# Optimization experiments

Hardware: AMD Instinct MI355X
Metric: run time of the kernel (lower is better)

Reference implementation:

```python
import jax, jax.numpy as jnp
import numpy as np

DIM = 512
HEADS = 8
DHEAD = 64
WIN = 128
QK_SCALE = 8.0
LN_EPS = 1e-5


def setup_inputs() -> dict:
    key = jax.random.key(0)
    ks = jax.random.split(key, 5)
    B, N = 8, 4096
    x = jax.random.normal(ks[0], (B, N, DIM), jnp.float32)
    w_qkv = jax.random.normal(ks[1], (3 * HEADS * DHEAD, DIM), jnp.float32) * 0.02
    w_out = jax.random.normal(ks[2], (DIM, HEADS * DHEAD), jnp.float32) * 0.02
    b_out = jnp.zeros((DIM,), jnp.float32)
    w_ff1 = jax.random.normal(ks[3], (4 * DIM, DIM), jnp.float32) * 0.02
    w_ff2 = jax.random.normal(ks[4], (DIM, 4 * DIM), jnp.float32) * 0.02
    return {
        'x': x, 'w_qkv': w_qkv,
        'q_scale': jnp.ones((DHEAD,), jnp.float32),
        'k_scale': jnp.ones((DHEAD,), jnp.float32),
        'w_out': w_out, 'b_out': b_out,
        'ln1_g': jnp.ones((DIM,), jnp.float32), 'ln1_b': jnp.zeros((DIM,), jnp.float32),
        'ff_ln_g': jnp.ones((DIM,), jnp.float32), 'ff_ln_b': jnp.zeros((DIM,), jnp.float32),
        'w_ff1': w_ff1, 'w_ff2': w_ff2,
    }


def _ln(x, g, b):
    m = jnp.mean(x, axis=-1, keepdims=True)
    v = jnp.mean((x - m) ** 2, axis=-1, keepdims=True)
    return (x - m) * jax.lax.rsqrt(v + LN_EPS) * g + b


def _l2norm(t):
    return t / jnp.clip(jnp.linalg.norm(t, axis=-1, keepdims=True), 1e-12)


def _rotary(t, pos):
    # t: (B, H, N, DHEAD); standard (non-xpos) rotary, half-split style
    inv_freq = 1.0 / (10000.0 ** (jnp.arange(0, DHEAD, 2, dtype=jnp.float32) / DHEAD))
    freqs = pos[:, None] * inv_freq                      # (N, DHEAD/2)
    emb = jnp.concatenate([freqs, freqs], axis=-1)       # (N, DHEAD)
    cos, sin = jnp.cos(emb), jnp.sin(emb)
    t1, t2 = t[..., : DHEAD // 2], t[..., DHEAD // 2:]
    rot = jnp.concatenate([-t2, t1], axis=-1)
    return t * cos + rot * sin


def reference(x, w_qkv, q_scale, k_scale, w_out, b_out, ln1_g, ln1_b,
              ff_ln_g, ff_ln_b, w_ff1, w_ff2):
    B, N, D = x.shape
    nw = N // WIN

    # ---- LocalMHA (prenorm, qk-rmsnorm, sliding window, causal) ----
    h = _ln(x, ln1_g, ln1_b)
    qkv = h @ w_qkv.T                                    # (B, N, 3*H*DHEAD)
    q, k, v = jnp.split(qkv, 3, axis=-1)

    def to_heads(t):
        return t.reshape(B, N, HEADS, DHEAD).transpose(0, 2, 1, 3)  # (B,H,N,d)

    q, k, v = to_heads(q), to_heads(k), to_heads(v)
    q = _l2norm(q) * q_scale
    k = _l2norm(k) * k_scale
    pos = jnp.arange(N, dtype=jnp.float32)
    q = _rotary(q, pos)
    k = _rotary(k, pos)

    # bucket into windows; keys/values look back one window
    bq = q.reshape(B, HEADS, nw, WIN, DHEAD)
    bk = k.reshape(B, HEADS, nw, WIN, DHEAD)
    bv = v.reshape(B, HEADS, nw, WIN, DHEAD)

    def look_back(t):
        prev = jnp.concatenate([jnp.zeros_like(t[:, :, :1]), t[:, :, :-1]], axis=2)
        return jnp.concatenate([prev, t], axis=3)

    kk, vv = look_back(bk), look_back(bv)

    qpos = jnp.arange(N, dtype=jnp.int32).reshape(nw, WIN)
    kprev = jnp.concatenate([jnp.full((1, WIN), -1, jnp.int32), qpos[:-1]], axis=0)
    kpos = jnp.concatenate([kprev, qpos], axis=1)
    mask = (qpos[:, :, None] >= kpos[:, None, :]) & (kpos[:, None, :] >= 0)

    sim = jnp.einsum('bhnid,bhnjd->bhnij', bq, kk) * QK_SCALE
    sim = jnp.where(mask, sim, -1e9)
    attn = jax.nn.softmax(sim, axis=-1)
    out = jnp.einsum('bhnij,bhnjd->bhnid', attn, vv)
    out = out.reshape(B, HEADS, N, DHEAD).transpose(0, 2, 1, 3).reshape(B, N, HEADS * DHEAD)
    x = x + out @ w_out.T + b_out

    # ---- FeedForward: LN -> Linear(4D, no bias) -> GELU -> Linear(D, no bias) ----
    hf = _ln(x, ff_ln_g, ff_ln_b)
    ff = jax.nn.gelu(hf @ w_ff1.T, approximate=False) @ w_ff2.T
    return x + ff
```

## Files before the change

kernel.cpp:

```cpp
#include <hip/hip_runtime.h>
#include <cstdint>
#include <cstddef>

typedef __bf16 bf16;
typedef __bf16 bf16x8 __attribute__((ext_vector_type(8)));
typedef float f32x4 __attribute__((ext_vector_type(4)));

#define DEV static __device__ __forceinline__

constexpr int BATCH = 8;
constexpr int SEQ = 4096;
constexpr int DIM = 512;
constexpr int HEADS = 8;
constexpr int DH = 64;
constexpr int WIN = 128;
constexpr int NW = SEQ / WIN;
constexpr int TOK = BATCH * SEQ;
constexpr float EPS = 1e-5f;

constexpr size_t R_EL   = (size_t)TOK * DIM;
constexpr size_t C_QKV  = 0;
constexpr size_t C_WOUT = 786432;
constexpr size_t C_WF1  = 1048576;
constexpr size_t C_WF2  = 2097152;
constexpr size_t C_SM   = 3145728;
constexpr size_t P_EL   = 3148416;

DEV void gload_lds16(const void* g, void* l) {
  __builtin_amdgcn_global_load_lds((__attribute__((address_space(1))) void*)g,
                                   (__attribute__((address_space(3))) void*)l,
                                   16, 0, 0);
}

DEV f32x4 mfma16(bf16x8 a, bf16x8 b, f32x4 c) {
  return __builtin_amdgcn_mfma_f32_16x16x32_bf16(a, b, c, 0, 0, 0);
}

struct SrcPtrs { const void* p[12]; };

DEV void copy8(const void* src, long si, bf16* dst, bool f32) {
  if (f32) {
    const float4* s = (const float4*)((const float*)src + si);
    float4 a = s[0], b = s[1];
    bf16x8 o;
    o[0] = (bf16)a.x; o[1] = (bf16)a.y; o[2] = (bf16)a.z; o[3] = (bf16)a.w;
    o[4] = (bf16)b.x; o[5] = (bf16)b.y; o[6] = (bf16)b.z; o[7] = (bf16)b.w;
    *(bf16x8*)dst = o;
  } else {
    *(bf16x8*)dst = *(const bf16x8*)((const bf16*)src + si);
  }
}

__global__ __launch_bounds__(256) void ingest_kernel(SrcPtrs sp, bf16* cano) {
  const bool f32 = (((const unsigned short*)sp.p[2])[0] == 0);
  const long e = (long)threadIdx.x * 8;
  int b = blockIdx.x;
  if (b < 384)  { long o = (long)b * 2048 + e; copy8(sp.p[1], o, cano + C_QKV + o, f32); return; }
  b -= 384;
  if (b < 128)  { long o = (long)b * 2048 + e; copy8(sp.p[4], o, cano + C_WOUT + o, f32); return; }
  b -= 128;
  if (b < 512)  { long o = (long)b * 2048 + e; copy8(sp.p[10], o, cano + C_WF1 + o, f32); return; }
  b -= 512;
  if (b < 512)  { long o = (long)b * 2048 + e; copy8(sp.p[11], o, cano + C_WF2 + o, f32); return; }
  b -= 512;
  const long o = (long)b * 2048 + e;
  if (o >= 2688) return;
  const void* src; long si;
  if      (o < 64)   { src = sp.p[2]; si = o; }
  else if (o < 128)  { src = sp.p[3]; si = o - 64; }
  else if (o < 640)  { src = sp.p[5]; si = o - 128; }
  else if (o < 1152) { src = sp.p[6]; si = o - 640; }
  else if (o < 1664) { src = sp.p[7]; si = o - 1152; }
  else if (o < 2176) { src = sp.p[8]; si = o - 1664; }
  else               { src = sp.p[9]; si = o - 2176; }
  copy8(src, si, cano + C_SM + o, f32);
}

__global__ __launch_bounds__(256) void ln_kernel(const void* __restrict__ in,
                                                 const bf16* __restrict__ gg,
                                                 const bf16* __restrict__ bb,
                                                 bf16* __restrict__ out,
                                                 const unsigned short* __restrict__ probe,
                                                 int raw) {
  const int wave = threadIdx.x >> 6, lane = threadIdx.x & 63;
  const int row = blockIdx.x * 4 + wave;
  const size_t base = (size_t)row * DIM + lane * 8;
  float f[8];
  if (raw && probe[0] == 0) {
    const float4* p = (const float4*)((const float*)in + base);
    float4 a = p[0], bq = p[1];
    f[0] = a.x; f[1] = a.y; f[2] = a.z; f[3] = a.w;
    f[4] = bq.x; f[5] = bq.y; f[6] = bq.z; f[7] = bq.w;
  } else {
    bf16x8 v = *(const bf16x8*)((const bf16*)in + base);
#pragma unroll
    for (int i = 0; i < 8; ++i) f[i] = (float)v[i];
  }
  float s = 0.f, sq = 0.f;
#pragma unroll
  for (int i = 0; i < 8; ++i) { s += f[i]; sq += f[i] * f[i]; }
#pragma unroll
  for (int m = 32; m; m >>= 1) { s += __shfl_xor(s, m); sq += __shfl_xor(sq, m); }
  const float mean = s * (1.0f / DIM);
  const float var = fmaxf(sq * (1.0f / DIM) - mean * mean, 0.0f);
  const float rs = rsqrtf(var + EPS);
  bf16x8 gv = *(const bf16x8*)(gg + lane * 8);
  bf16x8 bv = *(const bf16x8*)(bb + lane * 8);
  bf16x8 o;
#pragma unroll
  for (int i = 0; i < 8; ++i) o[i] = (bf16)((f[i] - mean) * rs * (float)gv[i] + (float)bv[i]);
  *(bf16x8*)((bf16*)out + base) = o;
}

template <int MODE>
__global__ __launch_bounds__(256) void gemm_bt(const bf16* __restrict__ A,
                                               const bf16* __restrict__ Bw,
                                               bf16* __restrict__ O0, bf16* __restrict__ O1,
                                               bf16* __restrict__ O2,
                                               float* __restrict__ Of,
                                               const void* __restrict__ Xraw,
                                               const bf16* __restrict__ Xb,
                                               const bf16* __restrict__ bias,
                                               const unsigned short* __restrict__ probe,
                                               int K, int bstride, int ostride, int gx) {
  __shared__ __align__(16) bf16 smem[2 * 128 * 32];
  bf16* As = smem;
  bf16* Bs = smem + 4096;
  const int tid = threadIdx.x;
  const int wave = tid >> 6, lane = tid & 63;
  const int l15 = lane & 15, quad = lane >> 4;
  const int id = blockIdx.x;
  const int per = gx * 8;
  const int tM = ((id / per) * 8 + (id & 7)) * 128;
  const int tN = ((id % per) >> 3) * 128;
  const int wM = (wave >> 1) * 64, wN = (wave & 1) * 64;
  f32x4 acc[4][4];
  const f32x4 z = {0.f, 0.f, 0.f, 0.f};
#pragma unroll
  for (int i = 0; i < 4; ++i)
#pragma unroll
    for (int j = 0; j < 4; ++j) acc[i][j] = z;

  for (int k0 = 0; k0 < K; k0 += 32) {
    __syncthreads();
#pragma unroll
    for (int t = 0; t < 2; ++t) {
      const int c = tid + t * 256;
      const int row = c >> 2, cc = (c & 3) * 8;
      gload_lds16(A + (size_t)(tM + row) * K + k0 + cc, &As[c * 8]);
      gload_lds16(Bw + (size_t)(tN + row) * bstride + k0 + cc, &Bs[c * 8]);
    }
    __syncthreads();
    bf16x8 aF[4], bF[4];
#pragma unroll
    for (int i = 0; i < 4; ++i) aF[i] = *(const bf16x8*)&As[(wM + i * 16 + l15) * 32 + quad * 8];
#pragma unroll
    for (int j = 0; j < 4; ++j) bF[j] = *(const bf16x8*)&Bs[(wN + j * 16 + l15) * 32 + quad * 8];
#pragma unroll
    for (int i = 0; i < 4; ++i)
#pragma unroll
      for (int j = 0; j < 4; ++j) acc[i][j] = mfma16(aF[i], bF[j], acc[i][j]);
  }

  if constexpr (MODE == 0) {
    __syncthreads();
    bf16* ob = smem + wave * 1152;
    const int colbase = tN + wN;
    const int which = colbase >> 9;
    const int head = (colbase >> 6) & 7;
    bf16* dst = which == 0 ? O0 : (which == 1 ? O1 : O2);
    const int ch = lane & 7;
    float scv[8], invf[8];
    if (which < 2) {
      const bf16* sc = which ? bias : Xb;
      bf16x8 s8 = *(const bf16x8*)(sc + ch * 8);
#pragma unroll
      for (int u = 0; u < 8; ++u) {
        scv[u] = (float)s8[u] * (which == 0 ? 8.0f : 1.0f);
        invf[u] = exp2f(-(float)((ch & 3) * 8 + u) * (13.287712379549449f / 32.0f));
      }
    }
#pragma unroll
    for (int i = 0; i < 4; ++i) {
#pragma unroll
      for (int j = 0; j < 4; ++j)
#pragma unroll
        for (int r = 0; r < 4; ++r)
          ob[(quad * 4 + r) * 72 + j * 16 + l15] = (bf16)acc[i][j][r];
#pragma unroll
      for (int t = 0; t < 2; ++t) {
        const int rr = t * 8 + (lane >> 3);
        const int rowg = tM + wM + i * 16 + rr;
        bf16x8 ov = *(const bf16x8*)&ob[rr * 72 + ch * 8];
        float f[8];
#pragma unroll
        for (int u = 0; u < 8; ++u) f[u] = (float)ov[u];
        if (which < 2) {
          float ss = 0.f;
#pragma unroll
          for (int u = 0; u < 8; ++u) ss += f[u] * f[u];
          ss += __shfl_xor(ss, 1); ss += __shfl_xor(ss, 2); ss += __shfl_xor(ss, 4);
          const float rs = 1.0f / fmaxf(sqrtf(ss), 1e-12f);
#pragma unroll
          for (int u = 0; u < 8; ++u) f[u] *= rs * scv[u];
          float pf[8];
#pragma unroll
          for (int u = 0; u < 8; ++u) pf[u] = __shfl_xor(f[u], 4);
          const float pos = (float)(rowg & (SEQ - 1));
#pragma unroll
          for (int u = 0; u < 8; ++u) {
            float sn, cs;
            __sincosf(pos * invf[u], &sn, &cs);
            const float rot = (ch < 4) ? -pf[u] : pf[u];
            f[u] = f[u] * cs + rot * sn;
          }
        }
        bf16x8 o8;
#pragma unroll
        for (int u = 0; u < 8; ++u) o8[u] = (bf16)f[u];
        const int bb = rowg >> 12, n = rowg & (SEQ - 1);
        *(bf16x8*)(dst + ((size_t)(bb * HEADS + head) * SEQ + n) * DH + ch * 8) = o8;
      }
    }
    return;
  }

  if constexpr (MODE == 1 || MODE == 2) {
    __syncthreads();
    bf16* ob = smem + wave * 1152;
    const int ch = lane & 7;
    bf16x8 bias8;
    bool xf32 = false;
    if constexpr (MODE == 1) {
      bias8 = *(const bf16x8*)(bias + tN + wN + ch * 8);
      xf32 = (probe[0] == 0);
    }
#pragma unroll
    for (int i = 0; i < 4; ++i) {
#pragma unroll
      for (int j = 0; j < 4; ++j)
#pragma unroll
        for (int r = 0; r < 4; ++r)
          ob[(quad * 4 + r) * 72 + j * 16 + l15] = (bf16)acc[i][j][r];
#pragma unroll
      for (int t = 0; t < 2; ++t) {
        const int rr = t * 8 + (lane >> 3);
        const int rowg = tM + wM + i * 16 + rr;
        bf16x8 ov = *(const bf16x8*)&ob[rr * 72 + ch * 8];
        bf16x8 o8;
        if constexpr (MODE == 1) {
          const size_t idx = (size_t)rowg * DIM + tN + wN + ch * 8;
          float xr[8];
          if (xf32) {
            const float4* xp = (const float4*)((const float*)Xraw + idx);
            float4 a = xp[0], bq = xp[1];
            xr[0] = a.x; xr[1] = a.y; xr[2] = a.z; xr[3] = a.w;
            xr[4] = bq.x; xr[5] = bq.y; xr[6] = bq.z; xr[7] = bq.w;
          } else {
            bf16x8 xv = *(const bf16x8*)((const bf16*)Xraw + idx);
#pragma unroll
            for (int u = 0; u < 8; ++u) xr[u] = (float)xv[u];
          }
#pragma unroll
          for (int u = 0; u < 8; ++u) o8[u] = (bf16)((float)ov[u] + xr[u] + (float)bias8[u]);
          *(bf16x8*)(O0 + idx) = o8;
        } else {
#pragma unroll
          for (int u = 0; u < 8; ++u) {
            const float v = (float)ov[u];
            o8[u] = (bf16)(0.5f * v * (1.0f + erff(v * 0.7071067811865476f)));
          }
          *(bf16x8*)(O0 + (size_t)rowg * ostride + tN + wN + ch * 8) = o8;
        }
      }
    }
    return;
  }

#pragma unroll
  for (int i = 0; i < 4; ++i) {
    const int rbase = tM + wM + i * 16 + quad * 4;
#pragma unroll
    for (int j = 0; j < 4; ++j) {
      const int col = tN + wN + j * 16 + l15;
#pragma unroll
      for (int r = 0; r < 4; ++r) {
        const int row = rbase + r;
        const float v = acc[i][j][r];
        if constexpr (MODE == 3) {
          const size_t idx = (size_t)row * DIM + col;
          Of[idx] = v + (float)Xb[idx];
        } else if constexpr (MODE == 4) {
          const size_t idx = (size_t)row * DIM + col;
          Of[idx] = v + Of[idx];
        }
      }
    }
  }
}

__global__ __launch_bounds__(256, 3) void attn_kernel(const bf16* __restrict__ q,
                                                      const bf16* __restrict__ k,
                                                      const bf16* __restrict__ v,
                                                      bf16* __restrict__ ao) {
  __shared__ __align__(16) bf16 kv[256 * 72];
  __shared__ __align__(16) bf16 pbuf[4][16 * 136];
  const int w = blockIdx.x, h = blockIdx.y, b = blockIdx.z;
  const int tid = threadIdx.x;
  const int wv = tid >> 6, lane = tid & 63;
  const int l15 = lane & 15, quad = lane >> 4;
  const size_t bh = (size_t)b * HEADS + h;
  const bf16* qb = q + bh * SEQ * DH;
  const bf16* kb = k + bh * SEQ * DH;
  const bf16* vb = v + bh * SEQ * DH;
  const int t0 = (w - 1) * WIN;

#pragma unroll
  for (int it = 0; it < 8; ++it) {
    const int c = it * 256 + tid;
    const int tok = c >> 3, ch = c & 7;
    int gt = t0 + tok; gt = gt < 0 ? 0 : gt;
    *(bf16x8*)&kv[tok * 72 + ch * 8] = *(const bf16x8*)(kb + (size_t)gt * DH + ch * 8);
  }
  bf16x8 aQ[2][2];
#pragma unroll
  for (int qt = 0; qt < 2; ++qt) {
    const int qtok = w * WIN + wv * 32 + qt * 16 + l15;
#pragma unroll
    for (int ks = 0; ks < 2; ++ks)
      aQ[qt][ks] = *(const bf16x8*)(qb + (size_t)qtok * DH + ks * 32 + quad * 8);
  }
  int gtv = t0 + tid; gtv = gtv < 0 ? 0 : gtv;
  bf16x8 vld[8];
#pragma unroll
  for (int dg = 0; dg < 8; ++dg)
    vld[dg] = *(const bf16x8*)(vb + (size_t)gtv * DH + dg * 8);
  __syncthreads();

  bf16x8 aP[2][8];
#pragma unroll
  for (int qt = 0; qt < 2; ++qt) {
    f32x4 sreg[16];
#pragma unroll
    for (int nt = 0; nt < 16; ++nt) {
      f32x4 a = {0.f, 0.f, 0.f, 0.f};
#pragma unroll
      for (int ks = 0; ks < 2; ++ks) {
        bf16x8 bK = *(const bf16x8*)&kv[(nt * 16 + l15) * 72 + ks * 32 + quad * 8];
        a = mfma16(aQ[qt][ks], bK, a);
      }
      sreg[nt] = a;
    }
    const int qlb = wv * 32 + qt * 16 + quad * 4;
    float rinv[4];
#pragma unroll
    for (int r = 0; r < 4; ++r) {
      const int ql = qlb + r;
      float sum = 0.f;
#pragma unroll
      for (int nt = 0; nt < 16; ++nt) {
        const int j = nt * 16 + l15;
        const bool valid = (nt < 8) ? (w > 0) : (ql >= j - WIN);
        const float p = valid ? __expf(sreg[nt][r]) : 0.0f;
        sreg[nt][r] = p;
        sum += p;
      }
#pragma unroll
      for (int m = 8; m; m >>= 1) sum += __shfl_xor(sum, m);
      rinv[r] = 1.0f / sum;
    }
#pragma unroll
    for (int half = 0; half < 2; ++half) {
#pragma unroll
      for (int ntw = 0; ntw < 8; ++ntw)
#pragma unroll
        for (int r = 0; r < 4; ++r)
          pbuf[wv][(quad * 4 + r) * 136 + ntw * 16 + l15] =
              (bf16)(sreg[half * 8 + ntw][r] * rinv[r]);
#pragma unroll
      for (int kk = 0; kk < 4; ++kk)
        aP[qt][half * 4 + kk] = *(const bf16x8*)&pbuf[wv][l15 * 136 + kk * 32 + quad * 8];
    }
  }
  __syncthreads();

#pragma unroll
  for (int dg = 0; dg < 8; ++dg)
#pragma unroll
    for (int i = 0; i < 8; ++i)
      kv[(dg * 8 + i) * 264 + tid] = vld[dg][i];
  __syncthreads();

#pragma unroll
  for (int qt = 0; qt < 2; ++qt) {
#pragma unroll
    for (int dt = 0; dt < 4; ++dt) {
      f32x4 o = {0.f, 0.f, 0.f, 0.f};
#pragma unroll
      for (int ks2 = 0; ks2 < 8; ++ks2) {
        bf16x8 bV = *(const bf16x8*)&kv[(dt * 16 + l15) * 264 + ks2 * 32 + quad * 8];
        o = mfma16(aP[qt][ks2], bV, o);
      }
#pragma unroll
      for (int r = 0; r < 4; ++r)
        pbuf[wv][(quad * 4 + r) * 136 + dt * 16 + l15] = (bf16)o[r];
    }
#pragma unroll
    for (int t = 0; t < 2; ++t) {
      const int rr = t * 8 + (lane >> 3), ch = lane & 7;
      bf16x8 ov = *(const bf16x8*)&pbuf[wv][rr * 136 + ch * 8];
      const int tok = w * WIN + wv * 32 + qt * 16 + rr;
      *(bf16x8*)(ao + ((size_t)b * SEQ + tok) * DIM + h * DH + ch * 8) = ov;
    }
  }
}

extern "C" void kernel_launch(void* const* d_in, const int* in_sizes, int n_in,
                              void* d_out, int out_size, void* d_ws, size_t ws_size,
                              hipStream_t stream) {
  (void)in_sizes; (void)n_in; (void)out_size;
  float* out = (float*)d_out;
  bf16* cano = (bf16*)d_ws;
  const unsigned short* probe = (const unsigned short*)d_in[2];

  SrcPtrs sp;
  for (int i = 0; i < 12; ++i) sp.p[i] = d_in[i];

  bf16* slot0 = cano + P_EL;
  bf16* slot1 = cano + P_EL + R_EL;
  bf16* slot2 = cano + P_EL + 2 * R_EL;
  bf16* slot3 = cano + P_EL + 3 * R_EL;

  const bf16* qsc  = cano + C_SM + 0;
  const bf16* ksc  = cano + C_SM + 64;
  const bf16* bout = cano + C_SM + 128;
  const bf16* l1g  = cano + C_SM + 640;
  const bf16* l1b  = cano + C_SM + 1152;
  const bf16* lfg  = cano + C_SM + 1664;
  const bf16* lfb  = cano + C_SM + 2176;

  ingest_kernel<<<1538, 256, 0, stream>>>(sp, cano);
  ln_kernel<<<TOK / 4, 256, 0, stream>>>(d_in[0], l1g, l1b, slot0, probe, 1);
  gemm_bt<0><<<12 * 256, 256, 0, stream>>>(slot0, cano + C_QKV, slot1, slot2, slot3,
                                           nullptr, nullptr, qsc, ksc, probe,
                                           DIM, DIM, 0, 12);
  attn_kernel<<<dim3(NW, HEADS, BATCH), 256, 0, stream>>>(slot1, slot2, slot3, slot0);
  gemm_bt<1><<<4 * 256, 256, 0, stream>>>(slot0, cano + C_WOUT, slot1, nullptr, nullptr,
                                          nullptr, d_in[0], nullptr, bout, probe,
                                          DIM, DIM, 0, 4);
  ln_kernel<<<TOK / 4, 256, 0, stream>>>(slot1, lfg, lfb, slot0, probe, 0);

  const bool big = ws_size >= (size_t)(P_EL + 6 * R_EL) * 2;
  if (big) {
    bf16* f1 = slot2;
    gemm_bt<2><<<16 * 256, 256, 0, stream>>>(slot0, cano + C_WF1, f1, nullptr, nullptr,
                                             nullptr, nullptr, nullptr, nullptr, probe,
                                             DIM, DIM, 2048, 16);
    gemm_bt<3><<<4 * 256, 256, 0, stream>>>(f1, cano + C_WF2, nullptr, nullptr, nullptr,
                                            out, nullptr, slot1, nullptr, probe,
                                            2048, 2048, 0, 4);
  } else {
    bf16* f1h = slot2;
    for (int half = 0; half < 2; ++half) {
      const bf16* w1h = cano + C_WF1 + (size_t)half * 1024 * DIM;
      const bf16* w2h = cano + C_WF2 + (size_t)half * 1024;
      gemm_bt<2><<<8 * 256, 256, 0, stream>>>(slot0, w1h, f1h, nullptr, nullptr,
                                              nullptr, nullptr, nullptr, nullptr, probe,
                                              DIM, DIM, 1024, 8);
      if (half == 0)
        gemm_bt<3><<<4 * 256, 256, 0, stream>>>(f1h, w2h, nullptr, nullptr, nullptr,
                                                out, nullptr, slot1, nullptr, probe,
                                                1024, 2048, 0, 4);
      else
        gemm_bt<4><<<4 * 256, 256, 0, stream>>>(f1h, w2h, nullptr, nullptr, nullptr,
                                                out, nullptr, nullptr, nullptr, probe,
                                                1024, 2048, 0, 4);
    }
  }
}
```

Before: 577.9 us.

## Double-buffer GEMM LDS tiles and vectorize fp32 residual epilogue via LDS staging

The GEMM main loop now ping-pongs between two LDS buffers, issuing global-to-LDS loads for the next K slice before computing on the current one, so memory latency overlaps with MFMA work and one barrier per iteration goes away. The fp32 epilogue modes (residual add into Of) now stage accumulators through LDS and emit 32-byte vectorized loads and stores instead of scattered scalar accesses. This doubles LDS use per block, which may reduce occupancy.

```diff
diff --git a/kernel.cpp b/kernel.cpp
--- a/kernel.cpp
+++ b/kernel.cpp
@@ -123,9 +123,7 @@
                                                const bf16* __restrict__ bias,
                                                const unsigned short* __restrict__ probe,
                                                int K, int bstride, int ostride, int gx) {
-  __shared__ __align__(16) bf16 smem[2 * 128 * 32];
-  bf16* As = smem;
-  bf16* Bs = smem + 4096;
+  __shared__ __align__(16) bf16 smem[4 * 128 * 32];
   const int tid = threadIdx.x;
   const int wave = tid >> 6, lane = tid & 63;
   const int l15 = lane & 15, quad = lane >> 4;
@@ -141,16 +139,25 @@
 #pragma unroll
     for (int j = 0; j < 4; ++j) acc[i][j] = z;
 
-  for (int k0 = 0; k0 < K; k0 += 32) {
-    __syncthreads();
+  auto stage = [&](int k0, int p) {
+    bf16* dA = smem + p * 8192;
+    bf16* dB = dA + 4096;
 #pragma unroll
     for (int t = 0; t < 2; ++t) {
       const int c = tid + t * 256;
       const int row = c >> 2, cc = (c & 3) * 8;
-      gload_lds16(A + (size_t)(tM + row) * K + k0 + cc, &As[c * 8]);
-      gload_lds16(Bw + (size_t)(tN + row) * bstride + k0 + cc, &Bs[c * 8]);
-    }
+      gload_lds16(A + (size_t)(tM + row) * K + k0 + cc, &dA[c * 8]);
+      gload_lds16(Bw + (size_t)(tN + row) * bstride + k0 + cc, &dB[c * 8]);
+    }
+  };
+
+  stage(0, 0);
+  int cur = 0;
+  for (int k0 = 0; k0 < K; k0 += 32) {
     __syncthreads();
+    if (k0 + 32 < K) stage(k0 + 32, cur ^ 1);
+    const bf16* As = smem + cur * 8192;
+    const bf16* Bs = As + 4096;
     bf16x8 aF[4], bF[4];
 #pragma unroll
     for (int i = 0; i < 4; ++i) aF[i] = *(const bf16x8*)&As[(wM + i * 16 + l15) * 32 + quad * 8];
@@ -160,6 +167,7 @@
     for (int i = 0; i < 4; ++i)
 #pragma unroll
       for (int j = 0; j < 4; ++j) acc[i][j] = mfma16(aF[i], bF[j], acc[i][j]);
+    cur ^= 1;
   }
 
   if constexpr (MODE == 0) {
@@ -277,25 +285,41 @@
     return;
   }
 
-#pragma unroll
-  for (int i = 0; i < 4; ++i) {
-    const int rbase = tM + wM + i * 16 + quad * 4;
-#pragma unroll
-    for (int j = 0; j < 4; ++j) {
-      const int col = tN + wN + j * 16 + l15;
-#pragma unroll
-      for (int r = 0; r < 4; ++r) {
-        const int row = rbase + r;
-        const float v = acc[i][j][r];
+  if constexpr (MODE == 3 || MODE == 4) {
+    __syncthreads();
+    float* obf = (float*)smem + wave * 1088;
+    const int ch = lane & 7;
+#pragma unroll
+    for (int i = 0; i < 4; ++i) {
+#pragma unroll
+      for (int j = 0; j < 4; ++j)
+#pragma unroll
+        for (int r = 0; r < 4; ++r)
+          obf[(quad * 4 + r) * 68 + j * 16 + l15] = acc[i][j][r];
+#pragma unroll
+      for (int t = 0; t < 2; ++t) {
+        const int rr = t * 8 + (lane >> 3);
+        const int rowg = tM + wM + i * 16 + rr;
+        const size_t idx = (size_t)rowg * DIM + tN + wN + ch * 8;
+        const float4* rp = (const float4*)&obf[rr * 68 + ch * 8];
+        float4 a = rp[0], b = rp[1];
+        float f[8] = {a.x, a.y, a.z, a.w, b.x, b.y, b.z, b.w};
         if constexpr (MODE == 3) {
-          const size_t idx = (size_t)row * DIM + col;
-          Of[idx] = v + (float)Xb[idx];
-        } else if constexpr (MODE == 4) {
-          const size_t idx = (size_t)row * DIM + col;
-          Of[idx] = v + Of[idx];
+          bf16x8 xv = *(const bf16x8*)(Xb + idx);
+#pragma unroll
+          for (int u = 0; u < 8; ++u) f[u] += (float)xv[u];
+        } else {
+          const float4* op = (const float4*)(Of + idx);
+          float4 oa = op[0], ob4 = op[1];
+          f[0] += oa.x; f[1] += oa.y; f[2] += oa.z; f[3] += oa.w;
+          f[4] += ob4.x; f[5] += ob4.y; f[6] += ob4.z; f[7] += ob4.w;
         }
-      }
-    }
+        float4 o0 = {f[0], f[1], f[2], f[3]}, o1 = {f[4], f[5], f[6], f[7]};
+        ((float4*)(Of + idx))[0] = o0;
+        ((float4*)(Of + idx))[1] = o1;
+      }
+    }
+    return;
   }
 }
 
```

After: 535.7 us. 1.08x faster.
